# Kernel optimization log

Hardware: AMD Instinct MI355X
Metric: run time of the kernel (lower is better)

Reference implementation:

```python
import math
import jax, jax.numpy as jnp
import numpy as np

B, S, D, H = 2, 2048, 1024, 16
HD = D // H  # 64
EPS = 1e-5


def _layernorm(x, g, b):
    mu = jnp.mean(x, axis=-1, keepdims=True)
    var = jnp.mean(jnp.square(x - mu), axis=-1, keepdims=True)
    return (x - mu) * jax.lax.rsqrt(var + EPS) * g + b


def setup_inputs() -> dict:
    key = jax.random.key(0)
    ks = jax.random.split(key, 16)
    s_attn = 1.0 / math.sqrt(D)
    s_mlp = 1.0 / math.sqrt(4 * D)
    return {
        "hidden_states": jax.random.normal(ks[0], (B, S, D), jnp.float32),
        # MHA params (torch Linear convention: y = x @ W.T + b)
        "Wqkv": jax.random.normal(ks[1], (3 * D, D), jnp.float32) * s_attn,
        "bqkv": jax.random.normal(ks[2], (3 * D,), jnp.float32) * s_attn,
        "Wout": jax.random.normal(ks[3], (D, D), jnp.float32) * s_attn,
        "bout": jax.random.normal(ks[4], (D,), jnp.float32) * s_attn,
        # LayerNorms
        "g1": jnp.ones((D,), jnp.float32),
        "b1": jnp.zeros((D,), jnp.float32),
        "g2": jnp.ones((D,), jnp.float32),
        "b2": jnp.zeros((D,), jnp.float32),
        # MLP (hidden = 4*D, activation = tanh)
        "W1": jax.random.normal(ks[5], (4 * D, D), jnp.float32) * s_attn,
        "bfc1": jax.random.normal(ks[6], (4 * D,), jnp.float32) * s_attn,
        "W2": jax.random.normal(ks[7], (D, 4 * D), jnp.float32) * s_mlp,
        "bfc2": jax.random.normal(ks[8], (D,), jnp.float32) * s_mlp,
    }


def _mha(x, Wqkv, bqkv, Wout, bout):
    # qkv: (B,S,3,H,hd)
    qkv = (x @ Wqkv.T + bqkv).reshape(B, S, 3, H, HD)
    q, k, v = qkv[:, :, 0], qkv[:, :, 1], qkv[:, :, 2]
    # NOTE: source einsum 'bshd,btjd->bsht' contracts over k's head axis j,
    # so each query head attends against sum-over-heads of K (and of V).
    k_sum = k.sum(axis=2)  # (B,S,hd)
    v_sum = v.sum(axis=2)  # (B,S,hd)
    scale = 1.0 / math.sqrt(HD)
    scores = jnp.einsum('bshd,btd->bsht', q, k_sum) * scale  # (B,S,H,S)
    causal = jnp.triu(jnp.ones((S, S), bool), k=1)  # True above diagonal
    scores = jnp.where(causal[None, :, None, :], -jnp.inf, scores)
    attn = jax.nn.softmax(scores, axis=-1)
    out = jnp.einsum('bsht,btd->bshd', attn, v_sum).reshape(B, S, D)
    return out @ Wout.T + bout


def reference(hidden_states, Wqkv, bqkv, Wout, bout, g1, b1, g2, b2, W1, bfc1, W2, bfc2):
    # eval mode: dropouts and stochastic-depth are identity
    residual = hidden_states
    h = _layernorm(residual, g1, b1)
    h = _mha(h, Wqkv, bqkv, Wout, bout)
    residual = h + residual
    h = _layernorm(residual, g2, b2)
    h = jnp.tanh(h @ W1.T + bfc1) @ W2.T + bfc2
    return (h, residual)
```

## Files before the change

### kernel.cpp

```cpp
#include <hip/hip_runtime.h>
#include <hip/hip_bf16.h>

typedef __attribute__((ext_vector_type(8))) short s16x8;
typedef __attribute__((ext_vector_type(4))) float f32x4;
typedef __hip_bfloat16 bf16_t;

__device__ __forceinline__ void gload_lds16(const void* g, void* l) {
  __builtin_amdgcn_global_load_lds(
      (__attribute__((address_space(1))) void*)(g),
      (__attribute__((address_space(3))) void*)(l), 16, 0, 0);
}

__device__ __forceinline__ unsigned cvt_pk_bf16(float lo, float hi) {
  unsigned r;
  asm("v_cvt_pk_bf16_f32 %0, %1, %2" : "=v"(r) : "v"(lo), "v"(hi));
  return r;
}

__device__ __forceinline__ float fast_tanh(float x) {
  float t = exp2f(x * 2.885390082f);
  return 1.0f - 2.0f * __builtin_amdgcn_rcpf(t + 1.0f);
}

__global__ void cast_all_k(const float* __restrict__ Wqkv, const float* __restrict__ Wout,
                           const float* __restrict__ W1, const float* __restrict__ W2,
                           bf16_t* __restrict__ Wqkv_bf, bf16_t* __restrict__ Wout_bf,
                           bf16_t* __restrict__ W1_bf, bf16_t* __restrict__ W2_bf) {
  int c = blockIdx.x * 256 + threadIdx.x;
  const float* src; bf16_t* dst; int off;
  if (c < 131072)      { src = Wqkv; dst = Wqkv_bf; off = c; }
  else if (c < 262144) { src = Wout; dst = Wout_bf; off = c - 131072; }
  else if (c < 786432) { src = W1;   dst = W1_bf;   off = c - 262144; }
  else                 { src = W2;   dst = W2_bf;   off = c - 786432; }
  int i = off * 8;
  float4 a = *(const float4*)(src + i);
  float4 b = *(const float4*)(src + i + 4);
  union { bf16_t h[8]; s16x8 v; } u;
  u.h[0] = __float2bfloat16(a.x); u.h[1] = __float2bfloat16(a.y);
  u.h[2] = __float2bfloat16(a.z); u.h[3] = __float2bfloat16(a.w);
  u.h[4] = __float2bfloat16(b.x); u.h[5] = __float2bfloat16(b.y);
  u.h[6] = __float2bfloat16(b.z); u.h[7] = __float2bfloat16(b.w);
  *(s16x8*)(dst + i) = u.v;
}

__global__ void reduce_kv_k(const float* __restrict__ Wqkv, bf16_t* __restrict__ Wred) {
  int d   = blockIdx.x & 63;
  int isv = blockIdx.x >> 6;
  int col = threadIdx.x * 4;
  const float* base = Wqkv + (size_t)(1024 + isv * 1024 + d) * 1024 + col;
  float4 s = {0.f, 0.f, 0.f, 0.f};
#pragma unroll
  for (int h = 0; h < 16; ++h) {
    float4 t = *(const float4*)(base + (size_t)h * 64 * 1024);
    s.x += t.x; s.y += t.y; s.z += t.z; s.w += t.w;
  }
  union { bf16_t h[4]; uint2 u; } o;
  o.h[0] = __float2bfloat16(s.x); o.h[1] = __float2bfloat16(s.y);
  o.h[2] = __float2bfloat16(s.z); o.h[3] = __float2bfloat16(s.w);
  *(uint2*)(Wred + (size_t)(isv * 64 + d) * 1024 + col) = o.u;
}

__global__ void bias_prep_k(const float* __restrict__ bqkv, float* __restrict__ br) {
  int i = blockIdx.x * 256 + threadIdx.x;
  if (i >= 1152) return;
  if (i < 1024) { br[i] = bqkv[i]; return; }
  int d = i - 1024;
  int off = (d < 64) ? (1024 + d) : (2048 + (d - 64));
  float s = 0.f;
#pragma unroll
  for (int h = 0; h < 16; ++h) s += bqkv[off + h * 64];
  br[i] = s;
}

__global__ __launch_bounds__(256) void ln_cast_k(const float* __restrict__ x,
                                                 const float* __restrict__ g,
                                                 const float* __restrict__ bb,
                                                 bf16_t* __restrict__ y) {
  int row = blockIdx.x, tid = threadIdx.x;
  float4 v = *(const float4*)(x + (size_t)row * 1024 + tid * 4);
  float s = v.x + v.y + v.z + v.w;
  float q = v.x * v.x + v.y * v.y + v.z * v.z + v.w * v.w;
#pragma unroll
  for (int off = 1; off < 64; off <<= 1) {
    s += __shfl_xor(s, off, 64);
    q += __shfl_xor(q, off, 64);
  }
  __shared__ float ss[4], qq[4];
  int wave = tid >> 6, lane = tid & 63;
  if (lane == 0) { ss[wave] = s; qq[wave] = q; }
  __syncthreads();
  s = ss[0] + ss[1] + ss[2] + ss[3];
  q = qq[0] + qq[1] + qq[2] + qq[3];
  float mu  = s * (1.0f / 1024.0f);
  float var = q * (1.0f / 1024.0f) - mu * mu;
  float rstd = rsqrtf(var + 1e-5f);
  float4 gg = *(const float4*)(g + tid * 4);
  float4 bv = *(const float4*)(bb + tid * 4);
  union { bf16_t h[4]; uint2 u; } o;
  o.h[0] = __float2bfloat16((v.x - mu) * rstd * gg.x + bv.x);
  o.h[1] = __float2bfloat16((v.y - mu) * rstd * gg.y + bv.y);
  o.h[2] = __float2bfloat16((v.z - mu) * rstd * gg.z + bv.z);
  o.h[3] = __float2bfloat16((v.w - mu) * rstd * gg.w + bv.w);
  *(uint2*)(y + (size_t)row * 1024 + tid * 4) = o.u;
}

template <int EPI>
__global__ __launch_bounds__(512) void gemm256(
    const bf16_t* __restrict__ A, const bf16_t* __restrict__ Bw,
    const float* __restrict__ bias, void* __restrict__ out0,
    int M, int N, int K, int Kslice) {
  __shared__ __align__(16) bf16_t As[3 * 8192];
  __shared__ __align__(16) bf16_t Bs[3 * 8192];
  const int tid  = threadIdx.x;
  const int lane = tid & 63;
  const int wave = tid >> 6;
  const int l15 = lane & 15, lg = lane >> 4;
  const int wm = wave >> 2, wn = wave & 3;
  const int bm = blockIdx.y * 256, bn = blockIdx.x * 256;
  const size_t Kz = (size_t)K;
  const int kstart = blockIdx.z * Kslice;
  const int srow = lane >> 2;
  const int scol = ((lane & 3) ^ ((lane >> 3) & 3)) * 8;
  const int rdoff = (lg ^ ((l15 >> 1) & 3)) * 8;

  f32x4 acc[8][4];
#pragma unroll
  for (int f = 0; f < 8; ++f)
#pragma unroll
    for (int g = 0; g < 4; ++g) acc[f][g] = (f32x4){0.f, 0.f, 0.f, 0.f};

  const bf16_t* Ab = A + (size_t)bm * Kz + kstart;
  const bf16_t* Bb = Bw + (size_t)bn * Kz + kstart;

  auto stage = [&](int t, int buf) {
    const int k0 = t * 32;
#pragma unroll
    for (int j = 0; j < 2; ++j) {
      const int blk = wave * 2 + j;
      gload_lds16(Ab + (size_t)(blk * 16 + srow) * Kz + k0 + scol, As + buf * 8192 + blk * 512);
      gload_lds16(Bb + (size_t)(blk * 16 + srow) * Kz + k0 + scol, Bs + buf * 8192 + blk * 512);
    }
  };

  const int NT = Kslice >> 5;
  stage(0, 0);
  stage(1, 1);
  int b0 = 0, b1 = 1, b2 = 2;
  for (int t = 0; t < NT; ++t) {
    if (t + 1 < NT) asm volatile("s_waitcnt vmcnt(4)" ::: "memory");
    else            asm volatile("s_waitcnt vmcnt(0)" ::: "memory");
    __builtin_amdgcn_s_barrier();
    if (t + 2 < NT) stage(t + 2, b2);
    s16x8 af[8], bfv[4];
#pragma unroll
    for (int f = 0; f < 8; ++f)
      af[f] = *(const s16x8*)&As[b0 * 8192 + (wm * 128 + f * 16 + l15) * 32 + rdoff];
#pragma unroll
    for (int g = 0; g < 4; ++g)
      bfv[g] = *(const s16x8*)&Bs[b0 * 8192 + (wn * 64 + g * 16 + l15) * 32 + rdoff];
    __builtin_amdgcn_s_setprio(1);
#pragma unroll
    for (int f = 0; f < 8; ++f)
#pragma unroll
      for (int g = 0; g < 4; ++g)
        acc[f][g] = __builtin_amdgcn_mfma_f32_16x16x32_bf16(af[f], bfv[g], acc[f][g], 0, 0, 0);
    __builtin_amdgcn_s_setprio(0);
    int tmp = b0; b0 = b1; b1 = b2; b2 = tmp;
  }

#pragma unroll
  for (int f = 0; f < 8; ++f) {
    const int row0 = bm + wm * 128 + f * 16 + lg * 4;
#pragma unroll
    for (int g = 0; g < 4; ++g) {
      const int col = bn + wn * 64 + g * 16 + l15;
      const float bcol = (EPI == 4) ? 0.f : bias[col];
#pragma unroll
      for (int r = 0; r < 4; ++r) {
        const int rw = row0 + r;
        float c = acc[f][g][r] + bcol;
        if constexpr (EPI == 2) {
          ((bf16_t*)out0)[(size_t)rw * N + col] = __float2bfloat16(fast_tanh(c));
        } else {
          ((bf16_t*)out0)[((size_t)blockIdx.z * M + rw) * N + col] = __float2bfloat16(c);
        }
      }
    }
  }
}

template <int EPI>
__global__ __launch_bounds__(256) void gemm64(
    const bf16_t* __restrict__ A, const bf16_t* __restrict__ Bw,
    const float* __restrict__ bias, void* __restrict__ out0,
    const float* __restrict__ resid, bf16_t* __restrict__ oks,
    bf16_t* __restrict__ ovt, int M, int N, int K) {
  __shared__ __align__(16) bf16_t As[2 * 64 * 32];
  __shared__ __align__(16) bf16_t Bs[2 * 128 * 32];
  const int tid  = threadIdx.x;
  const int lane = tid & 63;
  const int wave = tid >> 6;
  const int l15 = lane & 15, lg = lane >> 4;
  const int wr = (wave >> 1) * 32, wc = (wave & 1) * 64;
  const int bm = blockIdx.y * 64, bn = blockIdx.x * 128;
  const size_t Kz = (size_t)K;
  const int srow = lane >> 2;
  const int scol = ((lane & 3) ^ ((lane >> 3) & 3)) * 8;

  f32x4 acc[2][4];
#pragma unroll
  for (int m = 0; m < 2; ++m)
#pragma unroll
    for (int n = 0; n < 4; ++n) acc[m][n] = (f32x4){0.f, 0.f, 0.f, 0.f};

  const bf16_t* Ab = A + (size_t)bm * Kz;
  const bf16_t* Bb = Bw + (size_t)bn * Kz;

  auto stage = [&](int t, int buf) {
    const int k0 = t * 32;
    gload_lds16(Ab + (size_t)(wave * 16 + srow) * Kz + k0 + scol, As + buf * 2048 + wave * 512);
#pragma unroll
    for (int j = 0; j < 2; ++j) {
      const int cw = wave * 2 + j;
      gload_lds16(Bb + (size_t)(cw * 16 + srow) * Kz + k0 + scol, Bs + buf * 4096 + cw * 512);
    }
  };

  const int NT = K >> 5;
  const int rdoff = (lg ^ ((l15 >> 1) & 3)) * 8;
  stage(0, 0);
  __syncthreads();
  int buf = 0;
  for (int t = 0; t < NT; ++t) {
    if (t + 1 < NT) stage(t + 1, buf ^ 1);
    s16x8 af[2], bfv[4];
#pragma unroll
    for (int m = 0; m < 2; ++m)
      af[m] = *(const s16x8*)&As[buf * 2048 + (wr + m * 16 + l15) * 32 + rdoff];
#pragma unroll
    for (int n = 0; n < 4; ++n)
      bfv[n] = *(const s16x8*)&Bs[buf * 4096 + (wc + n * 16 + l15) * 32 + rdoff];
#pragma unroll
    for (int m = 0; m < 2; ++m)
#pragma unroll
      for (int n = 0; n < 4; ++n)
        acc[m][n] = __builtin_amdgcn_mfma_f32_16x16x32_bf16(af[m], bfv[n], acc[m][n], 0, 0, 0);
    __syncthreads();
    buf ^= 1;
  }

#pragma unroll
  for (int m = 0; m < 2; ++m) {
    const int row0 = bm + wr + m * 16 + lg * 4;
#pragma unroll
    for (int n = 0; n < 4; ++n) {
      const int col = bn + wc + n * 16 + l15;
      const float bcol = bias[col];
#pragma unroll
      for (int r = 0; r < 4; ++r) {
        const int rw = row0 + r;
        float c = acc[m][n][r] + bcol;
        if constexpr (EPI == 0) {
          if (col < 1024) {
            ((bf16_t*)out0)[(size_t)rw * 1024 + col] =
                __float2bfloat16(c * 0.1803368801f);
          } else if (col < 1088) {
            int d = col - 1024, b = rw >> 11, t = rw & 2047;
            oks[((size_t)(b << 11) + t) * 64 + d] = __float2bfloat16(c);
          } else {
            int d = col - 1088, b = rw >> 11, t = rw & 2047;
            ovt[((size_t)b * 64 + d) * 2048 + t] = __float2bfloat16(c);
          }
        } else {
          ((float*)out0)[(size_t)rw * N + col] = c + resid[(size_t)rw * N + col];
        }
      }
    }
  }
}

__global__ __launch_bounds__(256) void fc2_reduce_k(const bf16_t* __restrict__ p,
                                                    const float* __restrict__ bias,
                                                    float* __restrict__ out) {
  const size_t PL = (size_t)4096 * 1024;
  size_t i = ((size_t)blockIdx.x * 256 + threadIdx.x) * 8;
  float acc[8];
  {
    union { s16x8 v; bf16_t h[8]; } u;
    u.v = *(const s16x8*)(p + i);
#pragma unroll
    for (int j = 0; j < 8; ++j) acc[j] = __bfloat162float(u.h[j]);
  }
#pragma unroll
  for (int z = 1; z < 4; ++z) {
    union { s16x8 v; bf16_t h[8]; } u;
    u.v = *(const s16x8*)(p + z * PL + i);
#pragma unroll
    for (int j = 0; j < 8; ++j) acc[j] += __bfloat162float(u.h[j]);
  }
  const int col = (int)(i & 1023);
#pragma unroll
  for (int j = 0; j < 8; ++j) acc[j] += bias[col + j];
  *(float4*)(out + i)     = (float4){acc[0], acc[1], acc[2], acc[3]};
  *(float4*)(out + i + 4) = (float4){acc[4], acc[5], acc[6], acc[7]};
}


template <bool MASK>
__device__ __forceinline__ void attn_tile(
    int t0, int p, const s16x8 (&qf)[2],
    const bf16_t* __restrict__ Ks, const bf16_t* __restrict__ Vs,
    bf16_t* __restrict__ Pl, int l15, int lg,
    float& m_run, float& l_part, f32x4 (&ao)[4]) {
  const int sw7 = l15 & 7;

  f32x4 sc[4];
#pragma unroll
  for (int n = 0; n < 4; ++n) sc[n] = (f32x4){0.f, 0.f, 0.f, 0.f};
#pragma unroll
  for (int ks2 = 0; ks2 < 2; ++ks2) {
#pragma unroll
    for (int n = 0; n < 4; ++n) {
      s16x8 kf = *(const s16x8*)&Ks[(n * 16 + l15) * 64 + (((ks2 << 2) | lg) ^ sw7) * 8];
      sc[n] = __builtin_amdgcn_mfma_f32_16x16x32_bf16(kf, qf[ks2], sc[n], 0, 0, 0);
    }
  }

  float mx = -1e30f;
#pragma unroll
  for (int n = 0; n < 4; ++n) {
#pragma unroll
    for (int r = 0; r < 4; ++r) {
      float v = sc[n][r];
      if (MASK && (t0 + n * 16 + lg * 4 + r > p)) v = -1e30f;
      sc[n][r] = v;
      mx = fmaxf(mx, v);
    }
  }
  if (__any(mx > m_run + 11.5f)) {
    float mxf = fmaxf(mx, __shfl_xor(mx, 16, 64));
    mxf = fmaxf(mxf, __shfl_xor(mxf, 32, 64));
    float mn = fmaxf(m_run, mxf);
    float alpha = exp2f(m_run - mn);
    m_run = mn;
    l_part *= alpha;
#pragma unroll
    for (int r = 0; r < 4; ++r) {
      float ar = __shfl(alpha, lg * 4 + r, 64);
#pragma unroll
      for (int n2 = 0; n2 < 4; ++n2) ao[n2][r] *= ar;
    }
  }
#pragma unroll
  for (int n = 0; n < 4; ++n) {
    float e0 = exp2f(sc[n][0] - m_run);
    float e1 = exp2f(sc[n][1] - m_run);
    float e2 = exp2f(sc[n][2] - m_run);
    float e3 = exp2f(sc[n][3] - m_run);
    l_part += (e0 + e1) + (e2 + e3);
    uint2 d;
    d.x = cvt_pk_bf16(e0, e1);
    d.y = cvt_pk_bf16(e2, e3);
    *(uint2*)&Pl[l15 * 72 + n * 16 + lg * 4] = d;
  }
#pragma unroll
  for (int ks2 = 0; ks2 < 2; ++ks2) {
    s16x8 pa = *(const s16x8*)&Pl[l15 * 72 + ks2 * 32 + lg * 8];
#pragma unroll
    for (int n2 = 0; n2 < 4; ++n2) {
      s16x8 vf = *(const s16x8*)&Vs[(n2 * 16 + l15) * 64 + (((ks2 << 2) | lg) ^ sw7) * 8];
      ao[n2] = __builtin_amdgcn_mfma_f32_16x16x32_bf16(pa, vf, ao[n2], 0, 0, 0);
    }
  }
}

__global__ __launch_bounds__(512) void attn_k(const bf16_t* __restrict__ q,
                                              const bf16_t* __restrict__ ksp,
                                              const bf16_t* __restrict__ vtp,
                                              bf16_t* __restrict__ o) {
  __shared__ __align__(16) bf16_t Ks[3 * 4096];
  __shared__ __align__(16) bf16_t Vs[3 * 4096];
  __shared__ __align__(16) bf16_t Plds[8][16 * 72];
  const int tid = threadIdx.x, lane = tid & 63, wave = tid >> 6;
  const int l15 = lane & 15, lg = lane >> 4;
  const int grp = blockIdx.x >> 1;
  const int b   = blockIdx.x & 1;
  const int pbase = 2040 - 8 * grp;
  const int p = pbase + wave;

  const bf16_t* qb_b = q   + (size_t)b * 32768 * 64;
  const bf16_t* ksb  = ksp + (size_t)b * 2048 * 64;
  const bf16_t* vtb  = vtp + (size_t)b * 64 * 2048;
  bf16_t*       ob   = o   + (size_t)b * 32768 * 64;
  bf16_t* Pl = &Plds[wave][0];

  const int srow = lane >> 3;
  const int scol = lane & 7;
  const int grow = wave * 8 + srow;
  const int gcol = scol ^ (grow & 7);
  const bf16_t* ksrc0 = ksb + (size_t)grow * 64 + gcol * 8;
  const bf16_t* vsrc0 = vtb + (size_t)grow * 2048 + gcol * 8;

  auto stageKV = [&](int t, int buf) {
    const int t0 = t * 64;
    gload_lds16(ksrc0 + (size_t)t0 * 64, Ks + buf * 4096 + wave * 512);
    gload_lds16(vsrc0 + t0, Vs + buf * 4096 + wave * 512);
  };

  s16x8 qf[2];
  {
    const bf16_t* qptr = qb_b + (size_t)(16 * p + l15) * 64;
    qf[0] = *(const s16x8*)(qptr + lg * 8);
    qf[1] = *(const s16x8*)(qptr + 32 + lg * 8);
  }

  float m_run = -1e30f, l_part = 0.f;
  f32x4 ao[4];
#pragma unroll
  for (int n = 0; n < 4; ++n) ao[n] = (f32x4){0.f, 0.f, 0.f, 0.f};

  const int nst = (pbase + 71) >> 6;
  stageKV(0, 0);
  if (nst > 1) stageKV(1, 1);
  int b0 = 0, b1 = 1, b2 = 2;
  for (int tt = 0; tt < nst; ++tt) {
    if (tt + 1 < nst) asm volatile("s_waitcnt vmcnt(2)" ::: "memory");
    else              asm volatile("s_waitcnt vmcnt(0)" ::: "memory");
    __builtin_amdgcn_s_barrier();
    if (tt + 2 < nst) stageKV(tt + 2, b2);
    const int t0 = tt * 64;
    if (t0 <= p) {
      const bf16_t* Kc = Ks + b0 * 4096;
      const bf16_t* Vc = Vs + b0 * 4096;
      if (t0 + 63 <= p)
        attn_tile<false>(t0, p, qf, Kc, Vc, Pl, l15, lg, m_run, l_part, ao);
      else
        attn_tile<true>(t0, p, qf, Kc, Vc, Pl, l15, lg, m_run, l_part, ao);
    }
    int tmp = b0; b0 = b1; b1 = b2; b2 = tmp;
  }

  float l2 = l_part + __shfl_xor(l_part, 16, 64);
  l2 += __shfl_xor(l2, 32, 64);
  float rl[4];
#pragma unroll
  for (int r = 0; r < 4; ++r) rl[r] = 1.0f / __shfl(l2, lg * 4 + r, 64);
#pragma unroll
  for (int n2 = 0; n2 < 4; ++n2) {
#pragma unroll
    for (int r = 0; r < 4; ++r) {
      const int row = 16 * p + lg * 4 + r;
      ob[(size_t)row * 64 + n2 * 16 + l15] = __float2bfloat16(ao[n2][r] * rl[r]);
    }
  }
}

extern "C" void kernel_launch(void* const* d_in, const int* in_sizes, int n_in,
                              void* d_out, int out_size, void* d_ws, size_t ws_size,
                              hipStream_t stream) {
  (void)in_sizes; (void)n_in; (void)out_size; (void)ws_size;
  const float* hidden = (const float*)d_in[0];
  const float* Wqkv   = (const float*)d_in[1];
  const float* bqkv   = (const float*)d_in[2];
  const float* Wout   = (const float*)d_in[3];
  const float* bout   = (const float*)d_in[4];
  const float* g1     = (const float*)d_in[5];
  const float* b1     = (const float*)d_in[6];
  const float* g2     = (const float*)d_in[7];
  const float* b2     = (const float*)d_in[8];
  const float* W1     = (const float*)d_in[9];
  const float* bfc1   = (const float*)d_in[10];
  const float* W2     = (const float*)d_in[11];
  const float* bfc2   = (const float*)d_in[12];

  float* out_h   = (float*)d_out;
  float* out_res = out_h + (size_t)4096 * 1024;

  char* ws = (char*)d_ws;
  auto alloc = [&](size_t bytes) {
    char* p = ws;
    ws += (bytes + 255) & ~(size_t)255;
    return p;
  };
  bf16_t* X1      = (bf16_t*)alloc((size_t)4096 * 1024 * 2);
  bf16_t* Wqkv_bf = (bf16_t*)alloc((size_t)1152 * 1024 * 2);
  float*  bias_r  = (float*)alloc(1152 * 4);
  bf16_t* qb      = (bf16_t*)alloc((size_t)4096 * 1024 * 2);
  bf16_t* ksum    = (bf16_t*)alloc((size_t)2 * 2048 * 64 * 2);
  bf16_t* vT      = (bf16_t*)alloc((size_t)2 * 64 * 2048 * 2);
  bf16_t* Ob      = (bf16_t*)alloc((size_t)4096 * 1024 * 2);
  bf16_t* Wout_bf = (bf16_t*)alloc((size_t)1024 * 1024 * 2);
  bf16_t* X2      = (bf16_t*)alloc((size_t)4096 * 1024 * 2);
  bf16_t* W1_bf   = (bf16_t*)alloc((size_t)4096 * 1024 * 2);
  bf16_t* W2_bf   = (bf16_t*)alloc((size_t)1024 * 4096 * 2);
  bf16_t* H1      = (bf16_t*)alloc((size_t)4096 * 4096 * 2);
  bf16_t* fc2_part = (bf16_t*)d_ws;

  cast_all_k<<<5120, 256, 0, stream>>>(Wqkv, Wout, W1, W2, Wqkv_bf, Wout_bf, W1_bf, W2_bf);
  reduce_kv_k<<<128, 256, 0, stream>>>(Wqkv, Wqkv_bf + (size_t)1024 * 1024);
  bias_prep_k<<<5, 256, 0, stream>>>(bqkv, bias_r);

  ln_cast_k<<<4096, 256, 0, stream>>>(hidden, g1, b1, X1);
  gemm64<0><<<dim3(9, 64), 256, 0, stream>>>(X1, Wqkv_bf, bias_r, qb, nullptr, ksum, vT,
                                             4096, 1152, 1024);
  attn_k<<<512, 512, 0, stream>>>(qb, ksum, vT, Ob);
  gemm64<1><<<dim3(8, 64), 256, 0, stream>>>(Ob, Wout_bf, bout, out_res, hidden, nullptr,
                                             nullptr, 4096, 1024, 1024);
  ln_cast_k<<<4096, 256, 0, stream>>>(out_res, g2, b2, X2);
  gemm256<2><<<dim3(16, 16), 512, 0, stream>>>(X2, W1_bf, bfc1, H1, 4096, 4096, 1024, 1024);
  gemm256<4><<<dim3(4, 16, 4), 512, 0, stream>>>(H1, W2_bf, nullptr, fc2_part,
                                                 4096, 1024, 4096, 1024);
  fc2_reduce_k<<<2048, 256, 0, stream>>>(fc2_part, bfc2, out_h);
}
```

Measured before the change: 228.1 us.

## Restructure gemm256 to BK=64 double buffering with XCD-aware block remap

The 256x256 GEMM now stages 64-wide K tiles into two LDS buffers instead of 32-wide tiles into three. The staging layout uses a row-XOR swizzle over 8 chunks, and each tile is consumed in two MFMA halves. Block IDs are also remapped round-robin across the 8 XCDs so neighbouring tiles share L2. The goal is fewer barriers per K step and better cache locality. The trade-off is a shallower prefetch, because each step waits for vmcnt(0) and only one tile is in flight.

```diff
diff --git a/kernel.cpp b/kernel.cpp
--- a/kernel.cpp
+++ b/kernel.cpp
@@ -109,19 +109,25 @@
     const bf16_t* __restrict__ A, const bf16_t* __restrict__ Bw,
     const float* __restrict__ bias, void* __restrict__ out0,
     int M, int N, int K, int Kslice) {
-  __shared__ __align__(16) bf16_t As[3 * 8192];
-  __shared__ __align__(16) bf16_t Bs[3 * 8192];
+  __shared__ __align__(16) bf16_t As[2 * 16384];
+  __shared__ __align__(16) bf16_t Bs[2 * 16384];
   const int tid  = threadIdx.x;
   const int lane = tid & 63;
   const int wave = tid >> 6;
   const int l15 = lane & 15, lg = lane >> 4;
   const int wm = wave >> 2, wn = wave & 3;
-  const int bm = blockIdx.y * 256, bn = blockIdx.x * 256;
+
+  const unsigned nx = gridDim.x, ny = gridDim.y;
+  unsigned fid = (blockIdx.z * ny + blockIdx.y) * nx + blockIdx.x;
+  const unsigned nwg = nx * ny * gridDim.z;
+  fid = (fid & 7) * (nwg >> 3) + (fid >> 3);
+  const unsigned bxu = fid % nx;
+  const unsigned rem = fid / nx;
+  const unsigned byu = rem % ny;
+  const unsigned bzu = rem / ny;
+  const int bm = byu * 256, bn = bxu * 256;
   const size_t Kz = (size_t)K;
-  const int kstart = blockIdx.z * Kslice;
-  const int srow = lane >> 2;
-  const int scol = ((lane & 3) ^ ((lane >> 3) & 3)) * 8;
-  const int rdoff = (lg ^ ((l15 >> 1) & 3)) * 8;
+  const int kstart = bzu * Kslice;
 
   f32x4 acc[8][4];
 #pragma unroll
@@ -132,40 +138,51 @@
   const bf16_t* Ab = A + (size_t)bm * Kz + kstart;
   const bf16_t* Bb = Bw + (size_t)bn * Kz + kstart;
 
+  const int srow = (tid & 7);
   auto stage = [&](int t, int buf) {
-    const int k0 = t * 32;
-#pragma unroll
-    for (int j = 0; j < 2; ++j) {
-      const int blk = wave * 2 + j;
-      gload_lds16(Ab + (size_t)(blk * 16 + srow) * Kz + k0 + scol, As + buf * 8192 + blk * 512);
-      gload_lds16(Bb + (size_t)(blk * 16 + srow) * Kz + k0 + scol, Bs + buf * 8192 + blk * 512);
+    const int k0 = t * 64;
+#pragma unroll
+    for (int j = 0; j < 4; ++j) {
+      const int c   = j * 512 + tid;
+      const int row = c >> 3;
+      const int kc  = (c & 7) ^ (row & 7);
+      gload_lds16(Ab + (size_t)row * Kz + k0 + kc * 8,
+                  As + buf * 16384 + (j * 512 + wave * 64) * 8);
+      gload_lds16(Bb + (size_t)row * Kz + k0 + kc * 8,
+                  Bs + buf * 16384 + (j * 512 + wave * 64) * 8);
     }
   };
-
-  const int NT = Kslice >> 5;
+  (void)srow;
+
+  const int NT = Kslice >> 6;
   stage(0, 0);
-  stage(1, 1);
-  int b0 = 0, b1 = 1, b2 = 2;
+  int buf = 0;
   for (int t = 0; t < NT; ++t) {
-    if (t + 1 < NT) asm volatile("s_waitcnt vmcnt(4)" ::: "memory");
-    else            asm volatile("s_waitcnt vmcnt(0)" ::: "memory");
+    asm volatile("s_waitcnt vmcnt(0)" ::: "memory");
     __builtin_amdgcn_s_barrier();
-    if (t + 2 < NT) stage(t + 2, b2);
-    s16x8 af[8], bfv[4];
-#pragma unroll
-    for (int f = 0; f < 8; ++f)
-      af[f] = *(const s16x8*)&As[b0 * 8192 + (wm * 128 + f * 16 + l15) * 32 + rdoff];
-#pragma unroll
-    for (int g = 0; g < 4; ++g)
-      bfv[g] = *(const s16x8*)&Bs[b0 * 8192 + (wn * 64 + g * 16 + l15) * 32 + rdoff];
-    __builtin_amdgcn_s_setprio(1);
-#pragma unroll
-    for (int f = 0; f < 8; ++f)
-#pragma unroll
-      for (int g = 0; g < 4; ++g)
-        acc[f][g] = __builtin_amdgcn_mfma_f32_16x16x32_bf16(af[f], bfv[g], acc[f][g], 0, 0, 0);
-    __builtin_amdgcn_s_setprio(0);
-    int tmp = b0; b0 = b1; b1 = b2; b2 = tmp;
+    if (t + 1 < NT) stage(t + 1, buf ^ 1);
+#pragma unroll
+    for (int h = 0; h < 2; ++h) {
+      s16x8 af[8], bfv[4];
+#pragma unroll
+      for (int f = 0; f < 8; ++f) {
+        const int row = wm * 128 + f * 16 + l15;
+        af[f] = *(const s16x8*)&As[buf * 16384 + (row * 8 + ((h * 4 + lg) ^ (l15 & 7))) * 8];
+      }
+#pragma unroll
+      for (int g = 0; g < 4; ++g) {
+        const int row = wn * 64 + g * 16 + l15;
+        bfv[g] = *(const s16x8*)&Bs[buf * 16384 + (row * 8 + ((h * 4 + lg) ^ (l15 & 7))) * 8];
+      }
+      __builtin_amdgcn_s_setprio(1);
+#pragma unroll
+      for (int f = 0; f < 8; ++f)
+#pragma unroll
+        for (int g = 0; g < 4; ++g)
+          acc[f][g] = __builtin_amdgcn_mfma_f32_16x16x32_bf16(af[f], bfv[g], acc[f][g], 0, 0, 0);
+      __builtin_amdgcn_s_setprio(0);
+    }
+    buf ^= 1;
   }
 
 #pragma unroll
@@ -182,7 +199,7 @@
         if constexpr (EPI == 2) {
           ((bf16_t*)out0)[(size_t)rw * N + col] = __float2bfloat16(fast_tanh(c));
         } else {
-          ((bf16_t*)out0)[((size_t)blockIdx.z * M + rw) * N + col] = __float2bfloat16(c);
+          ((bf16_t*)out0)[((size_t)bzu * M + rw) * N + col] = __float2bfloat16(c);
         }
       }
     }
```

Result: faster. 212.6 us (-6.8%).
